# Kernel optimization log

Hardware: AMD Instinct MI355X
Metric: run time of the kernel (lower is better)

## Reference

```python
import jax, jax.numpy as jnp
import numpy as np

B, S, D, H = 2, 512, 1024, 8
DK = D // H
DFF = 4 * D
R = 51
SEP = 64


def setup_inputs() -> dict:
    key = jax.random.key(0)
    ks = jax.random.split(key, 12)
    def w(k, shape, scale=0.02):
        return jax.random.normal(k, shape, jnp.float32) * scale
    return {
        "x": jax.random.normal(ks[0], (B, S, D), jnp.float32),
        "relation": jax.random.randint(ks[1], (B, S, S), 0, R),
        "mask": jnp.ones((B, S, S), jnp.int32),
        "sep_id": SEP,
        "history_reg": jnp.ones((1,), jnp.float32),
        "Wq": w(ks[2], (D, D)), "bq": jnp.zeros((D,), jnp.float32),
        "Wk": w(ks[3], (D, D)), "bk": jnp.zeros((D,), jnp.float32),
        "Wv": w(ks[4], (D, D)), "bv": jnp.zeros((D,), jnp.float32),
        "Wo": w(ks[5], (D, D)), "bo": jnp.zeros((D,), jnp.float32),
        "rel_k_emb": w(ks[6], (R, DK)),
        "rel_v_emb": w(ks[7], (R, DK)),
        "ln1_g": jnp.ones((D,), jnp.float32), "ln1_b": jnp.zeros((D,), jnp.float32),
        "ln2_g": jnp.ones((D,), jnp.float32), "ln2_b": jnp.zeros((D,), jnp.float32),
        "W1": w(ks[8], (D, DFF)), "b1": jnp.zeros((DFF,), jnp.float32),
        "W2": w(ks[9], (DFF, D)), "b2": jnp.zeros((D,), jnp.float32),
    }


def _layer_norm(x, g, b, eps=1e-5):
    m = jnp.mean(x, axis=-1, keepdims=True)
    v = jnp.mean(jnp.square(x - m), axis=-1, keepdims=True)
    return (x - m) * jax.lax.rsqrt(v + eps) * g + b


def _forward(x, relation, mask, sep_id, history_reg, Wq, bq, Wk, bk, Wv, bv, Wo, bo,
             rel_k_emb, rel_v_emb, ln1_g, ln1_b, ln2_g, ln2_b, W1, b1, W2, b2):
    b, s, d = x.shape
    # relation-aware self-attention sublayer (pre-norm)
    h = _layer_norm(x, ln1_g, ln1_b)
    rk = rel_k_emb[relation]  # [B,S,S,DK]
    rv = rel_v_emb[relation]  # [B,S,S,DK]
    def proj(W, bias):
        return (h @ W + bias).reshape(b, s, H, DK).transpose(0, 2, 1, 3)  # [B,H,S,DK]
    q, k, v = proj(Wq, bq), proj(Wk, bk), proj(Wv, bv)
    scores = jnp.einsum("bhid,bhjd->bhij", q, k) + jnp.einsum("bhid,bijd->bhij", q, rk)
    scores = scores / jnp.sqrt(jnp.float32(DK))
    scores = jnp.where(mask[:, None, :, :] == 0, jnp.float32(-1e9), scores)
    attn = jax.nn.softmax(scores, axis=-1)  # [B,H,S,S]
    ctx = jnp.einsum("bhij,bhjd->bhid", attn, v) + jnp.einsum("bhij,bijd->bhid", attn, rv)
    ctx = ctx.transpose(0, 2, 1, 3).reshape(b, s, d)
    attn_out = ctx @ Wo + bo
    # history regularization loss: attention mass on history tokens (positions < sep_id)
    loss = history_reg[0] * jnp.mean(attn[:, :, :, :sep_id])
    x = x + attn_out
    # FFN sublayer (pre-norm)
    h2 = _layer_norm(x, ln2_g, ln2_b)
    ffn = jax.nn.relu(h2 @ W1 + b1) @ W2 + b2
    x = x + ffn
    return x, loss


def reference(x, relation, mask, sep_id, history_reg, Wq, bq, Wk, bk, Wv, bv, Wo, bo,
              rel_k_emb, rel_v_emb, ln1_g, ln1_b, ln2_g, ln2_b, W1, b1, W2, b2):
    return _forward(x, relation, mask, sep_id, history_reg, Wq, bq, Wk, bk, Wv, bv,
                    Wo, bo, rel_k_emb, rel_v_emb, ln1_g, ln1_b, ln2_g, ln2_b,
                    W1, b1, W2, b2)
```

## Files before the change

kernel.cpp:

```cpp
#include <hip/hip_runtime.h>
#include <hip/hip_bf16.h>

#define NB 2
#define NS 512
#define ND 1024
#define NH 8
#define NDK 128
#define NDFF 4096
#define RPAD 64
#define LDSC 640
#define BSROWS 1024
#define NBH 16

typedef __bf16 bf16x8 __attribute__((ext_vector_type(8)));
typedef __bf16 bf16x4 __attribute__((ext_vector_type(4)));
typedef float f32x4 __attribute__((ext_vector_type(4)));

#define BM 64
#define BN 64
#define BK 64

__device__ __forceinline__ void gload16(const void* g, void* l) {
    __builtin_amdgcn_global_load_lds(
        (const __attribute__((address_space(1))) void*)g,
        (__attribute__((address_space(3))) void*)l, 16, 0, 0);
}

__global__ __launch_bounds__(256, 4) void gemm64(
    const __bf16* __restrict__ A, const __bf16* __restrict__ Bt,
    const __bf16* __restrict__ Brel,
    float* __restrict__ Cf, __bf16* __restrict__ Cb,
    const float* __restrict__ bias,
    int Ksp, int lda, int ldb, int ldc,
    long sA, long sA2, int zdivA,
    long sB, long sB2, int zdivB,
    long sC, int nsplit, long sPart, int flags)
{
    __shared__ __bf16 As0[BM * BK];
    __shared__ __bf16 As1[BM * BK];
    __shared__ __bf16 Bs0[BN * BK];
    __shared__ __bf16 Bs1[BN * BK];

    const unsigned gx = gridDim.x, gy = gridDim.y;
    const unsigned n = gx * gy * gridDim.z;
    const unsigned o = blockIdx.x + gx * (blockIdx.y + gy * blockIdx.z);
    const unsigned q = n >> 3, r = n & 7, xcd = o & 7;
    const unsigned nl = (xcd < r ? xcd * (q + 1) : r * (q + 1) + (xcd - r) * q) + (o >> 3);
    const unsigned bx = nl % gx, tmp = nl / gx;
    const unsigned by = tmp % gy, bz = tmp / gy;

    const int z = bz;
    const int bh = z / nsplit, sp = z - bh * nsplit;
    const long kbase = (long)sp * Ksp;
    A  += (long)(bh / zdivA) * sA + (long)(bh % zdivA) * sA2 + kbase;
    Bt += (long)(bh / zdivB) * sB + (long)(bh % zdivB) * sB2 + kbase;
    const long cbase = (long)bh * sC + (long)sp * sPart;

    const int tM = by * BM, tN = bx * BN;
    const int t = threadIdx.x, lane = t & 63, w = t >> 6;
    const int wr = w >> 1, wc = w & 1;

    const __bf16* Bbase = Bt;
    int ldbx = ldb, tNB = tN;
    if ((flags & 4) && tN >= NS) { Bbase = Brel + kbase; ldbx = 128; tNB = tN - NS; }

    const int srow = lane >> 3;
    const int scolE = ((((lane & 7) << 4) ^ (srow << 4)) >> 1);

    const __bf16* gA = A + (long)(tM + srow) * lda + scolE;
    const __bf16* gB = Bbase + (long)(tNB + srow) * ldbx + scolE;

    f32x4 acc[2][2];
#pragma unroll
    for (int m = 0; m < 2; ++m)
#pragma unroll
        for (int nn = 0; nn < 2; ++nn)
#pragma unroll
            for (int j = 0; j < 4; ++j) acc[m][nn][j] = 0.f;

    const int r16 = lane & 15;
    const int kq = (lane >> 4) * 8;
    const int xorE = (r16 & 7) * 8;
    const int nt = Ksp / BK;

    auto STAGE = [&](__bf16* as, __bf16* bs, int k0) {
#pragma unroll
        for (int i = 0; i < 2; ++i) {
            const int rr = (w + i * 4) * 8;
            gload16(gA + (long)rr * lda + k0, (void*)&as[rr * BK]);
            gload16(gB + (long)rr * ldbx + k0, (void*)&bs[rr * BK]);
        }
    };
    auto COMPUTE = [&](const __bf16* as, const __bf16* bs) {
        __builtin_amdgcn_s_setprio(1);
#pragma unroll
        for (int ks = 0; ks < 2; ++ks) {
            bf16x8 af[2], bv[2];
#pragma unroll
            for (int m = 0; m < 2; ++m)
                af[m] = *(const bf16x8*)&as[(wr * 32 + m * 16 + r16) * BK + ((ks * 32 + kq) ^ xorE)];
#pragma unroll
            for (int nn = 0; nn < 2; ++nn)
                bv[nn] = *(const bf16x8*)&bs[(wc * 32 + nn * 16 + r16) * BK + ((ks * 32 + kq) ^ xorE)];
#pragma unroll
            for (int m = 0; m < 2; ++m)
#pragma unroll
                for (int nn = 0; nn < 2; ++nn)
                    acc[m][nn] = __builtin_amdgcn_mfma_f32_16x16x32_bf16(af[m], bv[nn], acc[m][nn], 0, 0, 0);
        }
        __builtin_amdgcn_s_setprio(0);
    };

    STAGE(As0, Bs0, 0);
    STAGE(As1, Bs1, BK);
    for (int tt = 0; tt < nt; tt += 2) {
        asm volatile("s_waitcnt vmcnt(4)\n\ts_barrier" ::: "memory");
        COMPUTE(As0, Bs0);
        asm volatile("s_waitcnt lgkmcnt(0)\n\ts_barrier" ::: "memory");
        const bool more = (tt + 2 < nt);
        if (more) {
            STAGE(As0, Bs0, (tt + 2) * BK);
            asm volatile("s_waitcnt vmcnt(4)\n\ts_barrier" ::: "memory");
        } else {
            asm volatile("s_waitcnt vmcnt(0)\n\ts_barrier" ::: "memory");
        }
        COMPUTE(As1, Bs1);
        asm volatile("s_waitcnt lgkmcnt(0)\n\ts_barrier" ::: "memory");
        if (more) STAGE(As1, Bs1, (tt + 3) * BK);
    }

    const bool relu = (flags & 1) != 0;
#pragma unroll
    for (int m = 0; m < 2; ++m) {
        const int gr0 = tM + wr * 32 + m * 16 + (lane >> 4) * 4;
#pragma unroll
        for (int nn = 0; nn < 2; ++nn) {
            const int gc = tN + wc * 32 + nn * 16 + (lane & 15);
            const float bb = bias ? bias[gc] : 0.f;
#pragma unroll
            for (int j = 0; j < 4; ++j) {
                float v = acc[m][nn][j] + bb;
                if (relu) v = fmaxf(v, 0.f);
                const long idx = cbase + (long)(gr0 + j) * ldc + gc;
                if (Cb) Cb[idx] = (__bf16)v;
                else Cf[idx] = v;
            }
        }
    }
}

__global__ void prep_weights(
    const float* __restrict__ Wq, const float* __restrict__ Wk,
    const float* __restrict__ Wv, const float* __restrict__ Wo,
    const float* __restrict__ W1, const float* __restrict__ W2,
    const float* __restrict__ relv,
    const float* __restrict__ bq, const float* __restrict__ bk,
    const float* __restrict__ bv, const float* __restrict__ relk,
    const float* __restrict__ x, const float* __restrict__ ln1g,
    const float* __restrict__ ln1b,
    __bf16* __restrict__ WqkvT, __bf16* __restrict__ WoT,
    __bf16* __restrict__ W1T, __bf16* __restrict__ W2T,
    __bf16* __restrict__ relvT, float* __restrict__ biasqkv,
    __bf16* __restrict__ relkT, __bf16* __restrict__ h1, int R)
{
    const int tile = blockIdx.x;
    const int t = threadIdx.y * 32 + threadIdx.x;

    if (tile >= 12372) {
        const long row = tile - 12372;
        const float* xr = x + row * ND;
        float4 v = reinterpret_cast<const float4*>(xr)[t];
        float s = v.x + v.y + v.z + v.w;
        float s2 = v.x * v.x + v.y * v.y + v.z * v.z + v.w * v.w;
#pragma unroll
        for (int o = 32; o > 0; o >>= 1) {
            s += __shfl_xor(s, o, 64);
            s2 += __shfl_xor(s2, o, 64);
        }
        __shared__ float red[8];
        const int lane = t & 63, wv = t >> 6;
        if (lane == 0) { red[wv] = s; red[4 + wv] = s2; }
        __syncthreads();
        s = red[0] + red[1] + red[2] + red[3];
        s2 = red[4] + red[5] + red[6] + red[7];
        const float mean = s * (1.f / ND);
        const float var = s2 * (1.f / ND) - mean * mean;
        const float rs = rsqrtf(var + 1e-5f);
        const float xv[4] = {v.x, v.y, v.z, v.w};
        bf16x4 o;
#pragma unroll
        for (int j = 0; j < 4; ++j) {
            const int c = t * 4 + j;
            o[j] = (__bf16)((xv[j] - mean) * rs * ln1g[c] + ln1b[c]);
        }
        *(bf16x4*)&h1[row * ND + t * 4] = o;
        return;
    }
    if (tile >= 12296) {
        const int ft = (tile - 12296) * 256 + t;
        if (ft < ND) biasqkv[ft] = bq[ft];
        else if (ft < 2 * ND) biasqkv[ft] = bk[ft - ND];
        else if (ft < 3 * ND) biasqkv[ft] = bv[ft - 2 * ND];
        else {
            const int idx = ft - 3 * ND;
            if (idx < 128 * NDK) {
                const int r = idx / NDK;
                relkT[idx] = (r < R) ? (__bf16)relk[idx] : (__bf16)0.f;
            }
        }
        return;
    }
    const float* src; __bf16* dst;
    int rows_in, cols_in, ldo, kx, ny;
    if (tile < 4096) {
        const int m = tile >> 10, r = tile & 1023;
        kx = r & 31; ny = r >> 5;
        rows_in = 1024; cols_in = 1024; ldo = 1024;
        src = m == 0 ? Wq : m == 1 ? Wk : m == 2 ? Wv : Wo;
        dst = m == 3 ? WoT : WqkvT + (size_t)m * 1024 * 1024;
    } else if (tile < 8192) {
        const int r = tile - 4096;
        kx = r & 31; ny = r >> 5;
        rows_in = 1024; cols_in = 4096; ldo = 1024; src = W1; dst = W1T;
    } else if (tile < 12288) {
        const int r = tile - 8192;
        kx = r & 127; ny = r >> 7;
        rows_in = 4096; cols_in = 1024; ldo = 4096; src = W2; dst = W2T;
    } else {
        const int r = tile - 12288;
        kx = r & 1; ny = r >> 1;
        rows_in = R; cols_in = 128; ldo = 64; src = relv; dst = relvT;
    }

    __shared__ float tl[32][33];
    const int k0 = kx * 32, n0 = ny * 32;
    const int tx = threadIdx.x, ty = threadIdx.y;
#pragma unroll
    for (int dy = 0; dy < 32; dy += 8) {
        const int k = k0 + ty + dy, nn = n0 + tx;
        tl[ty + dy][tx] = (k < rows_in && nn < cols_in) ? src[(long)k * cols_in + nn] : 0.f;
    }
    __syncthreads();
#pragma unroll
    for (int dy = 0; dy < 32; dy += 8) {
        const int nn = n0 + ty + dy, k = k0 + tx;
        if (nn < cols_in && k < ldo) dst[(long)nn * ldo + k] = (__bf16)tl[tx][ty + dy];
    }
}

__global__ void transpose_v(const __bf16* __restrict__ qkvb, __bf16* __restrict__ vt)
{
    __shared__ __bf16 tile[32][33];
    const int bh = blockIdx.z, b = bh >> 3, h = bh & 7;
    const int d0 = blockIdx.x * 32, i0 = blockIdx.y * 32;
    const int tx = threadIdx.x, ty = threadIdx.y;
    const __bf16* src = qkvb + 2 * ND + h * NDK;
#pragma unroll
    for (int dy = 0; dy < 32; dy += 8)
        tile[ty + dy][tx] = src[(long)(b * NS + i0 + ty + dy) * (3 * ND) + d0 + tx];
    __syncthreads();
#pragma unroll
    for (int dy = 0; dy < 32; dy += 8)
        vt[((long)bh * NDK + d0 + ty + dy) * NS + i0 + tx] = tile[tx][ty + dy];
}

__global__ __launch_bounds__(256) void softmax_rel(
    const __bf16* __restrict__ scores,
    const int* __restrict__ relation, const int* __restrict__ mask,
    __bf16* __restrict__ attn, __bf16* __restrict__ attnR,
    float* __restrict__ loss_part, const int* __restrict__ sep_p)
{
    const int i = blockIdx.x, b = blockIdx.y;
    const int t = threadIdx.x;
    const int* rrow = relation + ((long)b * NS + i) * NS;
    const int* mrow = mask + ((long)b * NS + i) * NS;
    const int r0 = rrow[t], r1 = rrow[t + 256];
    const int m0 = mrow[t], m1 = mrow[t + 256];
    const int sep = *sep_p;
    const int lane = t & 63, wv = t >> 6;

    __shared__ float qrl[RPAD];
    __shared__ float bins[RPAD];
    __shared__ float red[4];

    const float sc = 0.088388347648318447f;
    float lsum = 0.f;

#pragma unroll 1
    for (int h = 0; h < NH; ++h) {
        const long bh = (long)(b * NH + h);
        const __bf16* srow = scores + (bh * NS + i) * LDSC;
        __bf16* arow = attn + (bh * NS + i) * NS;
        __bf16* aRrow = attnR + (bh * NS + i) * RPAD;

        if (t < RPAD) { qrl[t] = (float)srow[NS + t]; bins[t] = 0.f; }
        __syncthreads();

        float v0 = ((float)srow[t] + qrl[r0]) * sc;
        float v1 = ((float)srow[t + 256] + qrl[r1]) * sc;
        if (m0 == 0) v0 = -1e9f;
        if (m1 == 0) v1 = -1e9f;

        float mx = fmaxf(v0, v1);
#pragma unroll
        for (int o = 32; o > 0; o >>= 1) mx = fmaxf(mx, __shfl_xor(mx, o, 64));
        if (lane == 0) red[wv] = mx;
        __syncthreads();
        mx = fmaxf(fmaxf(red[0], red[1]), fmaxf(red[2], red[3]));
        __syncthreads();

        const float e0 = __expf(v0 - mx), e1 = __expf(v1 - mx);
        float sm = e0 + e1;
#pragma unroll
        for (int o = 32; o > 0; o >>= 1) sm += __shfl_xor(sm, o, 64);
        if (lane == 0) red[wv] = sm;
        __syncthreads();
        sm = red[0] + red[1] + red[2] + red[3];

        const float inv = 1.f / sm;
        const float a0 = e0 * inv, a1 = e1 * inv;
        arow[t] = (__bf16)a0;
        arow[t + 256] = (__bf16)a1;
        atomicAdd(&bins[r0], a0);
        atomicAdd(&bins[r1], a1);
        if (t < sep) lsum += a0;
        if (t + 256 < sep) lsum += a1;
        __syncthreads();
        if (t < RPAD) aRrow[t] = (__bf16)bins[t];
        __syncthreads();
    }

#pragma unroll
    for (int o = 32; o > 0; o >>= 1) lsum += __shfl_xor(lsum, o, 64);
    if (lane == 0) red[wv] = lsum;
    __syncthreads();
    if (t == 0) loss_part[(long)b * NS + i] = red[0] + red[1] + red[2] + red[3];
}

__global__ __launch_bounds__(256) void ctx_reduce(
    const float* __restrict__ P, const __bf16* __restrict__ attnR,
    const __bf16* __restrict__ relvT, __bf16* __restrict__ ctxm)
{
    const int idx = blockIdx.x * 256 + threadIdx.x;
    const int d = idx & 127;
    const int i = (idx >> 7) & 511;
    const int h = (idx >> 16) & 7;
    const int b = idx >> 19;
    const long sP = (long)NBH * NS * NDK;
    float s = P[idx] + P[idx + sP];

    const bf16x8* ar = (const bf16x8*)(attnR + ((long)(idx >> 16) * NS + i) * RPAD);
    const bf16x8* rv = (const bf16x8*)(relvT + (long)d * RPAD);
    float acc = 0.f;
#pragma unroll
    for (int q = 0; q < 8; ++q) {
        bf16x8 a = ar[q], vv = rv[q];
#pragma unroll
        for (int j = 0; j < 8; ++j) acc += (float)a[j] * (float)vv[j];
    }
    ctxm[((long)(b * NS + i)) * ND + h * NDK + d] = (__bf16)(s + acc);
}

__global__ __launch_bounds__(256) void wo_reduce_ln(
    const float* __restrict__ P, const float* __restrict__ x,
    const float* __restrict__ bo, const float* __restrict__ g,
    const float* __restrict__ bb, float* __restrict__ out,
    __bf16* __restrict__ h2)
{
    const int row = blockIdx.x;
    const int t = threadIdx.x;
    const long i4 = (long)row * 256 + t;
    const long sP = (long)BSROWS * ND / 4;
    const float4* P4 = (const float4*)P;
    float4 s = P4[i4];
    const float4 t1 = P4[i4 + sP];
    s.x += t1.x; s.y += t1.y; s.z += t1.z; s.w += t1.w;
    const int col = t * 4;
    const float4 xv = ((const float4*)x)[i4];
    const float4 bv = *(const float4*)&bo[col];
    float4 o;
    o.x = s.x + xv.x + bv.x; o.y = s.y + xv.y + bv.y;
    o.z = s.z + xv.z + bv.z; o.w = s.w + xv.w + bv.w;
    ((float4*)out)[i4] = o;

    float sum = o.x + o.y + o.z + o.w;
    float sum2 = o.x * o.x + o.y * o.y + o.z * o.z + o.w * o.w;
#pragma unroll
    for (int of = 32; of > 0; of >>= 1) {
        sum += __shfl_xor(sum, of, 64);
        sum2 += __shfl_xor(sum2, of, 64);
    }
    __shared__ float red[8];
    const int lane = t & 63, wv = t >> 6;
    if (lane == 0) { red[wv] = sum; red[4 + wv] = sum2; }
    __syncthreads();
    sum = red[0] + red[1] + red[2] + red[3];
    sum2 = red[4] + red[5] + red[6] + red[7];
    const float mean = sum * (1.f / ND);
    const float var = sum2 * (1.f / ND) - mean * mean;
    const float rs = rsqrtf(var + 1e-5f);
    const float ov[4] = {o.x, o.y, o.z, o.w};
    bf16x4 hb;
#pragma unroll
    for (int j = 0; j < 4; ++j)
        hb[j] = (__bf16)((ov[j] - mean) * rs * g[col + j] + bb[col + j]);
    *(bf16x4*)&h2[(long)row * ND + col] = hb;
}

__global__ __launch_bounds__(256) void ffn2_reduce(
    const float* __restrict__ P, const float* __restrict__ b2, float* __restrict__ out,
    const float* __restrict__ loss_part, const float* __restrict__ hist,
    const int* __restrict__ sep_p, float* __restrict__ out_loss)
{
    const int i4 = blockIdx.x * 256 + threadIdx.x;
    const long sP = (long)BSROWS * ND / 4;
    const float4* P4 = (const float4*)P;
    float4 s = P4[i4];
    const float4 t1 = P4[i4 + sP];
    s.x += t1.x; s.y += t1.y; s.z += t1.z; s.w += t1.w;
    const int col = (i4 * 4) & (ND - 1);
    const float4 bv = *(const float4*)&b2[col];
    float4 o = ((float4*)out)[i4];
    o.x += s.x + bv.x; o.y += s.y + bv.y;
    o.z += s.z + bv.z; o.w += s.w + bv.w;
    ((float4*)out)[i4] = o;

    if (blockIdx.x == 0) {
        const int t = threadIdx.x;
        const float4 v = ((const float4*)loss_part)[t];
        float ls = v.x + v.y + v.z + v.w;
#pragma unroll
        for (int of = 32; of > 0; of >>= 1) ls += __shfl_xor(ls, of, 64);
        __shared__ float red[4];
        if ((t & 63) == 0) red[t >> 6] = ls;
        __syncthreads();
        if (t == 0) {
            const int sep = *sep_p;
            const float total = red[0] + red[1] + red[2] + red[3];
            const float denom = (float)NB * NH * NS * (float)(sep > 0 ? sep : 1);
            out_loss[0] = (sep > 0) ? hist[0] * total / denom : 0.f;
        }
    }
}

static inline int cdiv(int a, int b) { return (a + b - 1) / b; }

extern "C" void kernel_launch(void* const* d_in, const int* in_sizes, int n_in,
                              void* d_out, int out_size, void* d_ws, size_t ws_size,
                              hipStream_t stream)
{
    const float* x      = (const float*)d_in[0];
    const int* relation = (const int*)d_in[1];
    const int* mask     = (const int*)d_in[2];
    const int* sep_p    = (const int*)d_in[3];
    const float* hist   = (const float*)d_in[4];
    const float* Wq = (const float*)d_in[5],  *bq = (const float*)d_in[6];
    const float* Wk = (const float*)d_in[7],  *bk = (const float*)d_in[8];
    const float* Wv = (const float*)d_in[9],  *bv = (const float*)d_in[10];
    const float* Wo = (const float*)d_in[11], *bo = (const float*)d_in[12];
    const float* relk = (const float*)d_in[13];
    const float* relv = (const float*)d_in[14];
    const float* ln1g = (const float*)d_in[15], *ln1b = (const float*)d_in[16];
    const float* ln2g = (const float*)d_in[17], *ln2b = (const float*)d_in[18];
    const float* W1 = (const float*)d_in[19], *b1 = (const float*)d_in[20];
    const float* W2 = (const float*)d_in[21], *b2 = (const float*)d_in[22];
    const int R = in_sizes[13] / NDK;

    float* out = (float*)d_out;
    float* out_loss = out + (long)BSROWS * ND;

    char* p = (char*)d_ws;
    auto alloc = [&](size_t bytes) -> void* {
        void* r = (void*)p;
        p += (bytes + 255) & ~(size_t)255;
        return r;
    };
    __bf16* WqkvT   = (__bf16*)alloc((size_t)3 * ND * ND * 2);
    __bf16* WoT     = (__bf16*)alloc((size_t)ND * ND * 2);
    __bf16* W1T     = (__bf16*)alloc((size_t)NDFF * ND * 2);
    __bf16* W2T     = (__bf16*)alloc((size_t)ND * NDFF * 2);
    __bf16* relkT   = (__bf16*)alloc((size_t)128 * NDK * 2);
    __bf16* relvT   = (__bf16*)alloc((size_t)NDK * RPAD * 2);
    float*  biasqkv = (float*)alloc((size_t)3 * ND * 4);
    __bf16* h1      = (__bf16*)alloc((size_t)BSROWS * ND * 2);
    __bf16* qkvb    = (__bf16*)alloc((size_t)BSROWS * 3 * ND * 2);
    __bf16* vt      = (__bf16*)alloc((size_t)NBH * NDK * NS * 2);
    __bf16* attnb   = (__bf16*)alloc((size_t)NBH * NS * NS * 2);
    __bf16* attnR   = (__bf16*)alloc((size_t)NBH * NS * RPAD * 2);
    __bf16* ctxm    = (__bf16*)alloc((size_t)BSROWS * ND * 2);
    __bf16* h2      = (__bf16*)alloc((size_t)BSROWS * ND * 2);
    __bf16* F1      = (__bf16*)alloc((size_t)BSROWS * NDFF * 2);
    float*  loss_part = (float*)alloc((size_t)NB * NS * 4);
    float*  arena   = (float*)alloc((size_t)64 * 1024 * 1024);
    __bf16* scoresb = (__bf16*)arena;
    float* ctxPart  = arena + (size_t)3 * 1024 * 1024;
    float* woPart   = arena;
    float* f2Part   = arena + (size_t)2 * 1024 * 1024;

    const dim3 tb(32, 8);
    prep_weights<<<13396, tb, 0, stream>>>(Wq, Wk, Wv, Wo, W1, W2, relv,
                                           bq, bk, bv, relk, x, ln1g, ln1b,
                                           WqkvT, WoT, W1T, W2T, relvT,
                                           biasqkv, relkT, h1, R);

    gemm64<<<dim3(48, 16, 1), 256, 0, stream>>>(
        h1, WqkvT, nullptr, nullptr, qkvb, biasqkv,
        ND, ND, ND, 3 * ND,
        0, 0, 1, 0, 0, 1, 0, 1, 0, 0);

    transpose_v<<<dim3(4, 16, NBH), tb, 0, stream>>>(qkvb, vt);

    gemm64<<<dim3(10, 8, NBH), 256, 0, stream>>>(
        qkvb, qkvb + ND, relkT, nullptr, scoresb, nullptr,
        NDK, 3 * ND, 3 * ND, LDSC,
        (long)NS * 3 * ND, NDK, NH,
        (long)NS * 3 * ND, NDK, NH,
        (long)NS * LDSC, 1, 0, 4);

    softmax_rel<<<dim3(NS, NB), 256, 0, stream>>>(
        scoresb, relation, mask, attnb, attnR, loss_part, sep_p);

    gemm64<<<dim3(2, 8, NBH * 2), 256, 0, stream>>>(
        attnb, vt, nullptr, ctxPart, nullptr, nullptr,
        256, NS, NS, NDK,
        (long)NS * NS, 0, 1,
        (long)NDK * NS, 0, 1,
        (long)NS * NDK, 2, (long)NBH * NS * NDK, 0);

    ctx_reduce<<<4096, 256, 0, stream>>>(ctxPart, attnR, relvT, ctxm);

    gemm64<<<dim3(16, 16, 2), 256, 0, stream>>>(
        ctxm, WoT, nullptr, woPart, nullptr, nullptr,
        512, ND, ND, ND,
        0, 0, 1, 0, 0, 1,
        0, 2, (long)BSROWS * ND, 0);

    wo_reduce_ln<<<BSROWS, 256, 0, stream>>>(woPart, x, bo, ln2g, ln2b, out, h2);

    gemm64<<<dim3(64, 16, 1), 256, 0, stream>>>(
        h2, W1T, nullptr, nullptr, F1, b1,
        ND, ND, ND, NDFF,
        0, 0, 1, 0, 0, 1, 0, 1, 0, 1);

    gemm64<<<dim3(16, 16, 2), 256, 0, stream>>>(
        F1, W2T, nullptr, f2Part, nullptr, nullptr,
        2048, NDFF, NDFF, ND,
        0, 0, 1, 0, 0, 1,
        0, 2, (long)BSROWS * ND, 0);

    ffn2_reduce<<<1024, 256, 0, stream>>>(f2Part, b2, out,
                                          loss_part, hist, sep_p, out_loss);
}
```

Before: 162.2 us.

## Halve GEMM K-tile and fuse V transpose into QKV GEMM epilogue

The GEMM's K tile drops from 64 to 32, which halves LDS use per block. The staging layout, swizzle and waitcnt thresholds are reworked to match, and launch bounds now target 6 blocks per CU so occupancy can rise. The QKV projection epilogue now writes V straight into the transposed per-head layout, so the separate transpose_v kernel launch and its extra memory round trip are gone. In exchange, each K step does less work, so more barriers are needed per unit of compute, and the V stores are scattered 8-byte writes.

```diff
diff --git a/kernel.cpp b/kernel.cpp
--- a/kernel.cpp
+++ b/kernel.cpp
@@ -18,7 +18,7 @@
 
 #define BM 64
 #define BN 64
-#define BK 64
+#define BK 32
 
 __device__ __forceinline__ void gload16(const void* g, void* l) {
     __builtin_amdgcn_global_load_lds(
@@ -26,9 +26,9 @@
         (__attribute__((address_space(3))) void*)l, 16, 0, 0);
 }
 
-__global__ __launch_bounds__(256, 4) void gemm64(
+__global__ __launch_bounds__(256, 6) void gemm64(
     const __bf16* __restrict__ A, const __bf16* __restrict__ Bt,
-    const __bf16* __restrict__ Brel,
+    const __bf16* __restrict__ Brel, __bf16* __restrict__ vt,
     float* __restrict__ Cf, __bf16* __restrict__ Cb,
     const float* __restrict__ bias,
     int Ksp, int lda, int ldb, int ldc,
@@ -64,11 +64,11 @@
     int ldbx = ldb, tNB = tN;
     if ((flags & 4) && tN >= NS) { Bbase = Brel + kbase; ldbx = 128; tNB = tN - NS; }
 
-    const int srow = lane >> 3;
-    const int scolE = ((((lane & 7) << 4) ^ (srow << 4)) >> 1);
-
-    const __bf16* gA = A + (long)(tM + srow) * lda + scolE;
-    const __bf16* gB = Bbase + (long)(tNB + srow) * ldbx + scolE;
+    const int srow = lane >> 2;
+    const int scolE = ((((lane & 3) << 4) ^ ((srow & 3) << 4)) >> 1);
+
+    const __bf16* gA = A + (long)(tM + w * 16 + srow) * lda + scolE;
+    const __bf16* gB = Bbase + (long)(tNB + w * 16 + srow) * ldbx + scolE;
 
     f32x4 acc[2][2];
 #pragma unroll
@@ -80,47 +80,40 @@
 
     const int r16 = lane & 15;
     const int kq = (lane >> 4) * 8;
-    const int xorE = (r16 & 7) * 8;
+    const int xorE = (r16 & 3) * 8;
     const int nt = Ksp / BK;
 
     auto STAGE = [&](__bf16* as, __bf16* bs, int k0) {
-#pragma unroll
-        for (int i = 0; i < 2; ++i) {
-            const int rr = (w + i * 4) * 8;
-            gload16(gA + (long)rr * lda + k0, (void*)&as[rr * BK]);
-            gload16(gB + (long)rr * ldbx + k0, (void*)&bs[rr * BK]);
-        }
+        gload16(gA + k0, (void*)&as[w * 16 * BK]);
+        gload16(gB + k0, (void*)&bs[w * 16 * BK]);
     };
     auto COMPUTE = [&](const __bf16* as, const __bf16* bs) {
         __builtin_amdgcn_s_setprio(1);
-#pragma unroll
-        for (int ks = 0; ks < 2; ++ks) {
-            bf16x8 af[2], bv[2];
-#pragma unroll
-            for (int m = 0; m < 2; ++m)
-                af[m] = *(const bf16x8*)&as[(wr * 32 + m * 16 + r16) * BK + ((ks * 32 + kq) ^ xorE)];
+        bf16x8 af[2], bv[2];
+#pragma unroll
+        for (int m = 0; m < 2; ++m)
+            af[m] = *(const bf16x8*)&as[(wr * 32 + m * 16 + r16) * BK + (kq ^ xorE)];
+#pragma unroll
+        for (int nn = 0; nn < 2; ++nn)
+            bv[nn] = *(const bf16x8*)&bs[(wc * 32 + nn * 16 + r16) * BK + (kq ^ xorE)];
+#pragma unroll
+        for (int m = 0; m < 2; ++m)
 #pragma unroll
             for (int nn = 0; nn < 2; ++nn)
-                bv[nn] = *(const bf16x8*)&bs[(wc * 32 + nn * 16 + r16) * BK + ((ks * 32 + kq) ^ xorE)];
-#pragma unroll
-            for (int m = 0; m < 2; ++m)
-#pragma unroll
-                for (int nn = 0; nn < 2; ++nn)
-                    acc[m][nn] = __builtin_amdgcn_mfma_f32_16x16x32_bf16(af[m], bv[nn], acc[m][nn], 0, 0, 0);
-        }
+                acc[m][nn] = __builtin_amdgcn_mfma_f32_16x16x32_bf16(af[m], bv[nn], acc[m][nn], 0, 0, 0);
         __builtin_amdgcn_s_setprio(0);
     };
 
     STAGE(As0, Bs0, 0);
     STAGE(As1, Bs1, BK);
     for (int tt = 0; tt < nt; tt += 2) {
-        asm volatile("s_waitcnt vmcnt(4)\n\ts_barrier" ::: "memory");
+        asm volatile("s_waitcnt vmcnt(2)\n\ts_barrier" ::: "memory");
         COMPUTE(As0, Bs0);
         asm volatile("s_waitcnt lgkmcnt(0)\n\ts_barrier" ::: "memory");
         const bool more = (tt + 2 < nt);
         if (more) {
             STAGE(As0, Bs0, (tt + 2) * BK);
-            asm volatile("s_waitcnt vmcnt(4)\n\ts_barrier" ::: "memory");
+            asm volatile("s_waitcnt vmcnt(2)\n\ts_barrier" ::: "memory");
         } else {
             asm volatile("s_waitcnt vmcnt(0)\n\ts_barrier" ::: "memory");
         }
@@ -130,6 +123,7 @@
     }
 
     const bool relu = (flags & 1) != 0;
+    const bool vmode = (flags & 8) && (tN >= 2 * ND);
 #pragma unroll
     for (int m = 0; m < 2; ++m) {
         const int gr0 = tM + wr * 32 + m * 16 + (lane >> 4) * 4;
@@ -137,13 +131,22 @@
         for (int nn = 0; nn < 2; ++nn) {
             const int gc = tN + wc * 32 + nn * 16 + (lane & 15);
             const float bb = bias ? bias[gc] : 0.f;
-#pragma unroll
-            for (int j = 0; j < 4; ++j) {
-                float v = acc[m][nn][j] + bb;
-                if (relu) v = fmaxf(v, 0.f);
-                const long idx = cbase + (long)(gr0 + j) * ldc + gc;
-                if (Cb) Cb[idx] = (__bf16)v;
-                else Cf[idx] = v;
+            if (vmode) {
+                const int hd = gc - 2 * ND;
+                const int b = gr0 >> 9, i = gr0 & 511;
+                bf16x4 o;
+#pragma unroll
+                for (int j = 0; j < 4; ++j) o[j] = (__bf16)(acc[m][nn][j] + bb);
+                *(bf16x4*)&vt[(((long)b * NH + (hd >> 7)) * NDK + (hd & 127)) * NS + i] = o;
+            } else {
+#pragma unroll
+                for (int j = 0; j < 4; ++j) {
+                    float v = acc[m][nn][j] + bb;
+                    if (relu) v = fmaxf(v, 0.f);
+                    const long idx = cbase + (long)(gr0 + j) * ldc + gc;
+                    if (Cb) Cb[idx] = (__bf16)v;
+                    else Cf[idx] = v;
+                }
             }
         }
     }
@@ -246,22 +249,6 @@
         const int nn = n0 + ty + dy, k = k0 + tx;
         if (nn < cols_in && k < ldo) dst[(long)nn * ldo + k] = (__bf16)tl[tx][ty + dy];
     }
-}
-
-__global__ void transpose_v(const __bf16* __restrict__ qkvb, __bf16* __restrict__ vt)
-{
-    __shared__ __bf16 tile[32][33];
-    const int bh = blockIdx.z, b = bh >> 3, h = bh & 7;
-    const int d0 = blockIdx.x * 32, i0 = blockIdx.y * 32;
-    const int tx = threadIdx.x, ty = threadIdx.y;
-    const __bf16* src = qkvb + 2 * ND + h * NDK;
-#pragma unroll
-    for (int dy = 0; dy < 32; dy += 8)
-        tile[ty + dy][tx] = src[(long)(b * NS + i0 + ty + dy) * (3 * ND) + d0 + tx];
-    __syncthreads();
-#pragma unroll
-    for (int dy = 0; dy < 32; dy += 8)
-        vt[((long)bh * NDK + d0 + ty + dy) * NS + i0 + tx] = tile[tx][ty + dy];
 }
 
 __global__ __launch_bounds__(256) void softmax_rel(
@@ -504,14 +491,12 @@
                                            biasqkv, relkT, h1, R);
 
     gemm64<<<dim3(48, 16, 1), 256, 0, stream>>>(
-        h1, WqkvT, nullptr, nullptr, qkvb, biasqkv,
+        h1, WqkvT, nullptr, vt, nullptr, qkvb, biasqkv,
         ND, ND, ND, 3 * ND,
-        0, 0, 1, 0, 0, 1, 0, 1, 0, 0);
-
-    transpose_v<<<dim3(4, 16, NBH), tb, 0, stream>>>(qkvb, vt);
+        0, 0, 1, 0, 0, 1, 0, 1, 0, 8);
 
     gemm64<<<dim3(10, 8, NBH), 256, 0, stream>>>(
-        qkvb, qkvb + ND, relkT, nullptr, scoresb, nullptr,
+        qkvb, qkvb + ND, relkT, nullptr, nullptr, scoresb, nullptr,
         NDK, 3 * ND, 3 * ND, LDSC,
         (long)NS * 3 * ND, NDK, NH,
         (long)NS * 3 * ND, NDK, NH,
@@ -521,7 +506,7 @@
         scoresb, relation, mask, attnb, attnR, loss_part, sep_p);
 
     gemm64<<<dim3(2, 8, NBH * 2), 256, 0, stream>>>(
-        attnb, vt, nullptr, ctxPart, nullptr, nullptr,
+        attnb, vt, nullptr, nullptr, ctxPart, nullptr, nullptr,
         256, NS, NS, NDK,
         (long)NS * NS, 0, 1,
         (long)NDK * NS, 0, 1,
@@ -530,7 +515,7 @@
     ctx_reduce<<<4096, 256, 0, stream>>>(ctxPart, attnR, relvT, ctxm);
 
     gemm64<<<dim3(16, 16, 2), 256, 0, stream>>>(
-        ctxm, WoT, nullptr, woPart, nullptr, nullptr,
+        ctxm, WoT, nullptr, nullptr, woPart, nullptr, nullptr,
         512, ND, ND, ND,
         0, 0, 1, 0, 0, 1,
         0, 2, (long)BSROWS * ND, 0);
@@ -538,12 +523,12 @@
     wo_reduce_ln<<<BSROWS, 256, 0, stream>>>(woPart, x, bo, ln2g, ln2b, out, h2);
 
     gemm64<<<dim3(64, 16, 1), 256, 0, stream>>>(
-        h2, W1T, nullptr, nullptr, F1, b1,
+        h2, W1T, nullptr, nullptr, nullptr, F1, b1,
         ND, ND, ND, NDFF,
         0, 0, 1, 0, 0, 1, 0, 1, 0, 1);
 
     gemm64<<<dim3(16, 16, 2), 256, 0, stream>>>(
-        F1, W2T, nullptr, f2Part, nullptr, nullptr,
+        F1, W2T, nullptr, nullptr, f2Part, nullptr, nullptr,
         2048, NDFF, NDFF, ND,
         0, 0, 1, 0, 0, 1,
         0, 2, (long)BSROWS * ND, 0);
```

Result: slower. 172.9 us (+6.6%).

## Fuse V transpose into QKV GEMM epilogue and ctx reduction into attn·V GEMM

Applied to the files above, without the earlier changes.

The QKV GEMM epilogue now writes the V columns directly in transposed [b,h,d,s] layout, which removes the separate transpose_v kernel. The attn·V GEMM drops its split-K (K=512 in one pass) and adds the relative-value contribution (attnR·relvT) in its epilogue, writing bf16 ctxm directly. This eliminates the ctx_reduce kernel and the fp32 partial buffer round trip. In exchange, the attn·V grid shrinks to 256 blocks with twice the K loop, and the transposed V stores are strided 8-byte writes.

```diff
diff --git a/kernel.cpp b/kernel.cpp
--- a/kernel.cpp
+++ b/kernel.cpp
@@ -28,7 +28,9 @@
 
 __global__ __launch_bounds__(256, 4) void gemm64(
     const __bf16* __restrict__ A, const __bf16* __restrict__ Bt,
-    const __bf16* __restrict__ Brel,
+    const __bf16* __restrict__ Brel, __bf16* __restrict__ vt,
+    const __bf16* __restrict__ arP, const __bf16* __restrict__ rvP,
+    __bf16* __restrict__ ctxmP,
     float* __restrict__ Cf, __bf16* __restrict__ Cb,
     const float* __restrict__ bias,
     int Ksp, int lda, int ldb, int ldc,
@@ -129,7 +131,39 @@
         if (more) STAGE(As1, Bs1, (tt + 3) * BK);
     }
 
+    if (flags & 16) {
+        const int b = bh >> 3, h = bh & 7;
+#pragma unroll
+        for (int nn = 0; nn < 2; ++nn) {
+            const int gc = tN + wc * 32 + nn * 16 + (lane & 15);
+            bf16x8 rv[8];
+#pragma unroll
+            for (int qq = 0; qq < 8; ++qq)
+                rv[qq] = ((const bf16x8*)&rvP[(long)gc * RPAD])[qq];
+#pragma unroll
+            for (int m = 0; m < 2; ++m) {
+                const int gr0 = tM + wr * 32 + m * 16 + (lane >> 4) * 4;
+#pragma unroll
+                for (int j = 0; j < 4; ++j) {
+                    const int row = gr0 + j;
+                    const bf16x8* ar8 = (const bf16x8*)&arP[((long)bh * NS + row) * RPAD];
+                    float d = 0.f;
+#pragma unroll
+                    for (int qq = 0; qq < 8; ++qq) {
+                        const bf16x8 a = ar8[qq], vv = rv[qq];
+#pragma unroll
+                        for (int e = 0; e < 8; ++e) d += (float)a[e] * (float)vv[e];
+                    }
+                    ctxmP[((long)(b * NS + row)) * ND + h * NDK + gc] =
+                        (__bf16)(acc[m][nn][j] + d);
+                }
+            }
+        }
+        return;
+    }
+
     const bool relu = (flags & 1) != 0;
+    const bool vmode = (flags & 8) && (tN >= 2 * ND);
 #pragma unroll
     for (int m = 0; m < 2; ++m) {
         const int gr0 = tM + wr * 32 + m * 16 + (lane >> 4) * 4;
@@ -137,13 +171,22 @@
         for (int nn = 0; nn < 2; ++nn) {
             const int gc = tN + wc * 32 + nn * 16 + (lane & 15);
             const float bb = bias ? bias[gc] : 0.f;
-#pragma unroll
-            for (int j = 0; j < 4; ++j) {
-                float v = acc[m][nn][j] + bb;
-                if (relu) v = fmaxf(v, 0.f);
-                const long idx = cbase + (long)(gr0 + j) * ldc + gc;
-                if (Cb) Cb[idx] = (__bf16)v;
-                else Cf[idx] = v;
+            if (vmode) {
+                const int hd = gc - 2 * ND;
+                const int b = gr0 >> 9, i = gr0 & 511;
+                bf16x4 ov;
+#pragma unroll
+                for (int j = 0; j < 4; ++j) ov[j] = (__bf16)(acc[m][nn][j] + bb);
+                *(bf16x4*)&vt[(((long)b * NH + (hd >> 7)) * NDK + (hd & 127)) * NS + i] = ov;
+            } else {
+#pragma unroll
+                for (int j = 0; j < 4; ++j) {
+                    float v = acc[m][nn][j] + bb;
+                    if (relu) v = fmaxf(v, 0.f);
+                    const long idx = cbase + (long)(gr0 + j) * ldc + gc;
+                    if (Cb) Cb[idx] = (__bf16)v;
+                    else Cf[idx] = v;
+                }
             }
         }
     }
@@ -248,22 +291,6 @@
     }
 }
 
-__global__ void transpose_v(const __bf16* __restrict__ qkvb, __bf16* __restrict__ vt)
-{
-    __shared__ __bf16 tile[32][33];
-    const int bh = blockIdx.z, b = bh >> 3, h = bh & 7;
-    const int d0 = blockIdx.x * 32, i0 = blockIdx.y * 32;
-    const int tx = threadIdx.x, ty = threadIdx.y;
-    const __bf16* src = qkvb + 2 * ND + h * NDK;
-#pragma unroll
-    for (int dy = 0; dy < 32; dy += 8)
-        tile[ty + dy][tx] = src[(long)(b * NS + i0 + ty + dy) * (3 * ND) + d0 + tx];
-    __syncthreads();
-#pragma unroll
-    for (int dy = 0; dy < 32; dy += 8)
-        vt[((long)bh * NDK + d0 + ty + dy) * NS + i0 + tx] = tile[tx][ty + dy];
-}
-
 __global__ __launch_bounds__(256) void softmax_rel(
     const __bf16* __restrict__ scores,
     const int* __restrict__ relation, const int* __restrict__ mask,
@@ -335,30 +362,6 @@
     if (lane == 0) red[wv] = lsum;
     __syncthreads();
     if (t == 0) loss_part[(long)b * NS + i] = red[0] + red[1] + red[2] + red[3];
-}
-
-__global__ __launch_bounds__(256) void ctx_reduce(
-    const float* __restrict__ P, const __bf16* __restrict__ attnR,
-    const __bf16* __restrict__ relvT, __bf16* __restrict__ ctxm)
-{
-    const int idx = blockIdx.x * 256 + threadIdx.x;
-    const int d = idx & 127;
-    const int i = (idx >> 7) & 511;
-    const int h = (idx >> 16) & 7;
-    const int b = idx >> 19;
-    const long sP = (long)NBH * NS * NDK;
-    float s = P[idx] + P[idx + sP];
-
-    const bf16x8* ar = (const bf16x8*)(attnR + ((long)(idx >> 16) * NS + i) * RPAD);
-    const bf16x8* rv = (const bf16x8*)(relvT + (long)d * RPAD);
-    float acc = 0.f;
-#pragma unroll
-    for (int q = 0; q < 8; ++q) {
-        bf16x8 a = ar[q], vv = rv[q];
-#pragma unroll
-        for (int j = 0; j < 8; ++j) acc += (float)a[j] * (float)vv[j];
-    }
-    ctxm[((long)(b * NS + i)) * ND + h * NDK + d] = (__bf16)(s + acc);
 }
 
 __global__ __launch_bounds__(256) void wo_reduce_ln(
@@ -493,7 +496,6 @@
     float*  loss_part = (float*)alloc((size_t)NB * NS * 4);
     float*  arena   = (float*)alloc((size_t)64 * 1024 * 1024);
     __bf16* scoresb = (__bf16*)arena;
-    float* ctxPart  = arena + (size_t)3 * 1024 * 1024;
     float* woPart   = arena;
     float* f2Part   = arena + (size_t)2 * 1024 * 1024;
 
@@ -504,14 +506,14 @@
                                            biasqkv, relkT, h1, R);
 
     gemm64<<<dim3(48, 16, 1), 256, 0, stream>>>(
-        h1, WqkvT, nullptr, nullptr, qkvb, biasqkv,
+        h1, WqkvT, nullptr, vt, nullptr, nullptr, nullptr,
+        nullptr, qkvb, biasqkv,
         ND, ND, ND, 3 * ND,
-        0, 0, 1, 0, 0, 1, 0, 1, 0, 0);
-
-    transpose_v<<<dim3(4, 16, NBH), tb, 0, stream>>>(qkvb, vt);
+        0, 0, 1, 0, 0, 1, 0, 1, 0, 8);
 
     gemm64<<<dim3(10, 8, NBH), 256, 0, stream>>>(
-        qkvb, qkvb + ND, relkT, nullptr, scoresb, nullptr,
+        qkvb, qkvb + ND, relkT, nullptr, nullptr, nullptr, nullptr,
+        nullptr, scoresb, nullptr,
         NDK, 3 * ND, 3 * ND, LDSC,
         (long)NS * 3 * ND, NDK, NH,
         (long)NS * 3 * ND, NDK, NH,
@@ -520,17 +522,17 @@
     softmax_rel<<<dim3(NS, NB), 256, 0, stream>>>(
         scoresb, relation, mask, attnb, attnR, loss_part, sep_p);
 
-    gemm64<<<dim3(2, 8, NBH * 2), 256, 0, stream>>>(
-        attnb, vt, nullptr, ctxPart, nullptr, nullptr,
-        256, NS, NS, NDK,
+    gemm64<<<dim3(2, 8, NBH), 256, 0, stream>>>(
+        attnb, vt, nullptr, nullptr, attnR, relvT, ctxm,
+        nullptr, nullptr, nullptr,
+        NS, NS, NS, NDK,
         (long)NS * NS, 0, 1,
         (long)NDK * NS, 0, 1,
-        (long)NS * NDK, 2, (long)NBH * NS * NDK, 0);
-
-    ctx_reduce<<<4096, 256, 0, stream>>>(ctxPart, attnR, relvT, ctxm);
+        0, 1, 0, 16);
 
     gemm64<<<dim3(16, 16, 2), 256, 0, stream>>>(
-        ctxm, WoT, nullptr, woPart, nullptr, nullptr,
+        ctxm, WoT, nullptr, nullptr, nullptr, nullptr, nullptr,
+        woPart, nullptr, nullptr,
         512, ND, ND, ND,
         0, 0, 1, 0, 0, 1,
         0, 2, (long)BSROWS * ND, 0);
@@ -538,12 +540,14 @@
     wo_reduce_ln<<<BSROWS, 256, 0, stream>>>(woPart, x, bo, ln2g, ln2b, out, h2);
 
     gemm64<<<dim3(64, 16, 1), 256, 0, stream>>>(
-        h2, W1T, nullptr, nullptr, F1, b1,
+        h2, W1T, nullptr, nullptr, nullptr, nullptr, nullptr,
+        nullptr, F1, b1,
         ND, ND, ND, NDFF,
         0, 0, 1, 0, 0, 1, 0, 1, 0, 1);
 
     gemm64<<<dim3(16, 16, 2), 256, 0, stream>>>(
-        F1, W2T, nullptr, f2Part, nullptr, nullptr,
+        F1, W2T, nullptr, nullptr, nullptr, nullptr, nullptr,
+        f2Part, nullptr, nullptr,
         2048, NDFF, NDFF, ND,
         0, 0, 1, 0, 0, 1,
         0, 2, (long)BSROWS * ND, 0);
```

Result: no change. 159.2 us (-1.9%).
